# Kernel optimization log

Measured on AMD Instinct MI355X. Metric: run time of the kernel, lower is better.

Reference implementation:

```python
import jax, jax.numpy as jnp
import numpy as np

B, T, C, H = 4, 2048, 1024, 16
D = C // H  # head_size = 64


def setup_inputs() -> dict:
    key = jax.random.key(0)
    k1, k2, k3 = jax.random.split(key, 3)
    h = jax.random.normal(k1, (B, T, C), dtype=jnp.float32)
    # additive float mask, [B,1,1,T]; zeros = no padding
    attention_mask = jnp.zeros((B, 1, 1, T), dtype=jnp.float32)
    # learned params (bias=False linears), scaled like default torch init
    w_attn = jax.random.normal(k2, (C, 3 * C), dtype=jnp.float32) / np.sqrt(C)
    w_proj = jax.random.normal(k3, (C, C), dtype=jnp.float32) / np.sqrt(C)
    return {"h": h, "attention_mask": attention_mask, "w_attn": w_attn, "w_proj": w_proj}


def reference(h, attention_mask, w_attn, w_proj):
    # fused QKV projection: [B,T,3C]
    qkv = jnp.einsum("btc,cd->btd", h, w_attn)
    q, k, v = jnp.split(qkv, 3, axis=-1)
    # [B,T,C] -> [B,H,T,D]
    def to_heads(x):
        return x.reshape(B, T, H, D).transpose(0, 2, 1, 3)
    q, k, v = to_heads(q), to_heads(k), to_heads(v)
    # scaled dot-product attention with additive mask (non-causal)
    scale = 1.0 / np.sqrt(D).astype(np.float32)
    scores = jnp.einsum("bhqd,bhkd->bhqk", q, k) * scale + attention_mask
    probs = jax.nn.softmax(scores, axis=-1)
    y = jnp.einsum("bhqk,bhkd->bhqd", probs, v)
    # [B,H,T,D] -> [B,T,C]
    y = y.transpose(0, 2, 1, 3).reshape(B, T, C)
    return jnp.einsum("btc,cd->btd", y, w_proj)
```

## Files before the change

### kernel.cpp

```cpp
#include <hip/hip_runtime.h>
#include <hip/hip_bf16.h>

#define DEV static __device__ __forceinline__

typedef __attribute__((ext_vector_type(4))) float f32x4;
typedef __attribute__((ext_vector_type(8))) short bf16x8;

constexpr int Bb = 4, Ts = 2048, Cc = 1024, Hh = 16, Dd = 64;
constexpr int Mm = Bb * Ts;
constexpr float SCQ = 0.18033688f;

union frag_u {
  bf16x8 f;
  uint2  u2[2];
  ushort us[8];
  uint4  u4;
};

DEV ushort f2bf(float x) {
  union { float f; unsigned u; } v; v.f = x;
  unsigned r = v.u + 0x7FFFu + ((v.u >> 16) & 1u);
  return (ushort)(r >> 16);
}

DEV ushort f2bf_hw(float x) {
  union { __hip_bfloat16 b; ushort u; } cv;
  cv.b = __float2bfloat16(x);
  return cv.u;
}

typedef const __attribute__((address_space(1))) unsigned int gu32;
typedef __attribute__((address_space(3))) unsigned int lu32;
DEV void gload16(const void* g, void* l) {
  __builtin_amdgcn_global_load_lds((gu32*)g, (lu32*)l, 16, 0, 0);
}

DEV void ld_frag16(frag_u& fr, const ushort* lds, int row, int chunk) {
  int off = row * 128 + ((chunk ^ (row & 7)) << 4);
  fr.u4 = *reinterpret_cast<const uint4*>(reinterpret_cast<const char*>(lds) + off);
}
DEV void lds_st64p(ushort* lds, int row, int p, uint2 v) {
  int off = row * 128 + ((((p >> 3) ^ (row & 7)) << 4) | ((2 * p) & 15));
  *reinterpret_cast<uint2*>(reinterpret_cast<char*>(lds) + off) = v;
}

__global__ __launch_bounds__(256) void cvt_kernel(const float* __restrict__ in,
                                                  ushort* __restrict__ out, int n4) {
  for (int i = blockIdx.x * blockDim.x + threadIdx.x; i < n4;
       i += gridDim.x * blockDim.x) {
    float4 v = reinterpret_cast<const float4*>(in)[i];
    ushort4 o;
    o.x = f2bf(v.x); o.y = f2bf(v.y); o.z = f2bf(v.z); o.w = f2bf(v.w);
    reinterpret_cast<ushort4*>(out)[i] = o;
  }
}

__global__ __launch_bounds__(256) void transpose_cvt(const float* __restrict__ in,
                                                     ushort* __restrict__ out,
                                                     int R, int Ccols) {
  __shared__ float tile[32][33];
  int c0 = blockIdx.x * 32, r0 = blockIdx.y * 32;
  int tx = threadIdx.x & 31, ty = threadIdx.x >> 5;
#pragma unroll
  for (int i = 0; i < 4; ++i) {
    int r = ty + i * 8;
    tile[r][tx] = in[(size_t)(r0 + r) * Ccols + c0 + tx];
  }
  __syncthreads();
#pragma unroll
  for (int i = 0; i < 4; ++i) {
    int r = ty + i * 8;
    out[(size_t)(c0 + r) * R + r0 + tx] = f2bf(tile[tx][r]);
  }
}

__global__ __launch_bounds__(512, 2) void gemm256_qkv(const ushort* __restrict__ A,
                                                      const ushort* __restrict__ Bt,
                                                      ushort* __restrict__ Qb,
                                                      ushort* __restrict__ Kb,
                                                      ushort* __restrict__ Vb,
                                                      const float* __restrict__ maskp) {
  __shared__ ushort Lds[2][4][128 * 64];
  const int tid = threadIdx.x;
  const int lane = tid & 63, wid = tid >> 6;
  const int g = lane >> 4, l15 = lane & 15;
  const int wm = wid >> 2, wn = wid & 3;

  const int flat = blockIdx.y * 12 + blockIdx.x;
  const int swz = (flat & 7) * 48 + (flat >> 3);
  const int bx = swz % 12, by = swz / 12;
  const int m0 = by * 256, n0 = bx * 256;
  constexpr int K = 1024, nkt = K / 64;

#define STAGE(slot, region, gbase, gRow0, kt)                                   \
  {                                                                             \
    _Pragma("unroll") for (int i = 0; i < 2; ++i) {                             \
      int q = wid * 128 + i * 64 + lane;                                        \
      int row = q >> 3, c = (q & 7) ^ (row & 7);                                \
      gload16((gbase) + (size_t)((gRow0) + row) * K + (kt) * 64 + c * 8,        \
              &Lds[slot][region][(size_t)(wid * 128 + i * 64) * 8]);            \
    }                                                                           \
  }

  f32x4 acc[8][4];
#pragma unroll
  for (int i = 0; i < 8; ++i)
#pragma unroll
    for (int j = 0; j < 4; ++j) acc[i][j] = f32x4{0.f, 0.f, 0.f, 0.f};

  STAGE(0, 0, A, m0, 0);
  STAGE(0, 1, A, m0 + 128, 0);
  STAGE(0, 2, Bt, n0, 0);
  STAGE(0, 3, Bt, n0 + 128, 0);
  STAGE(1, 2, Bt, n0, 1);
  STAGE(1, 3, Bt, n0 + 128, 1);
  asm volatile("s_waitcnt vmcnt(4)" ::: "memory");
  __builtin_amdgcn_s_barrier();

  frag_u bf[4][2];
  for (int t = 0; t < nkt; ++t) {
    const int s = t & 1;
    const ushort* Acur = Lds[s][wm];
    const ushort* Bcur = Lds[s][2 + (wn >> 1)];
    const int browb = (wn & 1) * 64;

#pragma unroll
    for (int p = 0; p < 4; ++p) {
      frag_u af[2][2];
#pragma unroll
      for (int m2 = 0; m2 < 2; ++m2)
#pragma unroll
        for (int ks = 0; ks < 2; ++ks)
          ld_frag16(af[m2][ks], Acur, (2 * p + m2) * 16 + l15, 4 * ks + g);
      if (p == 0) {
#pragma unroll
        for (int n = 0; n < 4; ++n)
#pragma unroll
          for (int ks = 0; ks < 2; ++ks)
            ld_frag16(bf[n][ks], Bcur, browb + n * 16 + l15, 4 * ks + g);
        if (t + 1 < nkt) STAGE((t + 1) & 1, 0, A, m0, t + 1);
      }
      if (p == 1 && t + 2 < nkt) STAGE(s, 2, Bt, n0, t + 2);
      if (p == 2 && t + 1 < nkt) STAGE((t + 1) & 1, 1, A, m0 + 128, t + 1);
      if (p == 3 && t + 2 < nkt) STAGE(s, 3, Bt, n0 + 128, t + 2);

      __builtin_amdgcn_s_barrier();
      asm volatile("s_waitcnt lgkmcnt(0)" ::: "memory");
      __builtin_amdgcn_sched_barrier(0);
      __builtin_amdgcn_s_setprio(1);
#pragma unroll
      for (int m2 = 0; m2 < 2; ++m2)
#pragma unroll
        for (int n = 0; n < 4; ++n)
#pragma unroll
          for (int ks = 0; ks < 2; ++ks)
            acc[2 * p + m2][n] = __builtin_amdgcn_mfma_f32_16x16x32_bf16(
                af[m2][ks].f, bf[n][ks].f, acc[2 * p + m2][n], 0, 0, 0);
      __builtin_amdgcn_s_setprio(0);
      __builtin_amdgcn_sched_barrier(0);
      if (p == 3) asm volatile("s_waitcnt vmcnt(2)" ::: "memory");
      __builtin_amdgcn_s_barrier();
    }
  }
#undef STAGE

  asm volatile("s_waitcnt vmcnt(0)" ::: "memory");

  const int seg = bx >> 2;
  ushort* dst = (seg == 0) ? Qb : (seg == 1) ? Kb : Vb;
#pragma unroll
  for (int mi = 0; mi < 8; ++mi) {
#pragma unroll
    for (int r = 0; r < 4; ++r) {
      int mrow = m0 + wm * 128 + mi * 16 + 4 * g + r;
      int b = mrow >> 11, tt = mrow & 2047;
      float vs = (seg == 2) ? __expf(maskp[(size_t)b * Ts + tt])
                            : (seg == 0 ? SCQ : 1.f);
#pragma unroll
      for (int n = 0; n < 4; ++n) {
        int col = (bx & 3) * 256 + wn * 64 + n * 16 + l15;
        int hd = col >> 6, d = col & 63;
        size_t idx = (seg == 2)
            ? (((size_t)(b * Hh + hd)) * Dd + d) * Ts + tt
            : (((size_t)(b * Hh + hd)) * Ts + tt) * Dd + d;
        dst[idx] = f2bf(acc[mi][n][r] * vs);
      }
    }
  }
}

__global__ __launch_bounds__(256) void gemm_bt(const ushort* __restrict__ A,
                                               const ushort* __restrict__ Bt,
                                               int M, int N, int K,
                                               float* __restrict__ Cf) {
  __shared__ ushort Al[2][128 * 64];
  __shared__ ushort Bl[2][128 * 64];
  const int tid = threadIdx.x;
  const int lane = tid & 63, wid = tid >> 6;
  const int g = lane >> 4, l15 = lane & 15;
  const int wr = wid >> 1, wc = wid & 1;
  const int m0 = blockIdx.y * 128, n0 = blockIdx.x * 128;

#define ISSUE(slot, kt)                                                         \
  {                                                                             \
    _Pragma("unroll") for (int it = 0; it < 4; ++it) {                          \
      int chunk = wid * 256 + it * 64 + lane;                                   \
      int row = chunk >> 3, c16 = (chunk & 7) ^ (row & 7);                      \
      gload16(A + (size_t)(m0 + row) * K + (kt) * 64 + c16 * 8,                 \
              Al[slot] + (size_t)(wid * 256 + it * 64) * 8);                    \
      gload16(Bt + (size_t)(n0 + row) * K + (kt) * 64 + c16 * 8,                \
              Bl[slot] + (size_t)(wid * 256 + it * 64) * 8);                    \
    }                                                                           \
  }

  f32x4 acc[4][4];
#pragma unroll
  for (int i = 0; i < 4; ++i)
#pragma unroll
    for (int j = 0; j < 4; ++j) acc[i][j] = f32x4{0.f, 0.f, 0.f, 0.f};

  const int nkt = K >> 6;
  ISSUE(0, 0);
  __syncthreads();
  for (int kt = 0; kt < nkt; ++kt) {
    const int s = kt & 1;
    if (kt + 1 < nkt) ISSUE(s ^ 1, kt + 1);
#pragma unroll
    for (int ks = 0; ks < 2; ++ks) {
      frag_u af[4], bfr[4];
#pragma unroll
      for (int i = 0; i < 4; ++i) {
        ld_frag16(af[i], Al[s], wr * 64 + i * 16 + l15, 4 * ks + g);
        ld_frag16(bfr[i], Bl[s], wc * 64 + i * 16 + l15, 4 * ks + g);
      }
#pragma unroll
      for (int i = 0; i < 4; ++i)
#pragma unroll
        for (int j = 0; j < 4; ++j)
          acc[i][j] = __builtin_amdgcn_mfma_f32_16x16x32_bf16(af[i].f, bfr[j].f,
                                                              acc[i][j], 0, 0, 0);
    }
    __syncthreads();
  }
#undef ISSUE

#pragma unroll
  for (int i = 0; i < 4; ++i)
#pragma unroll
    for (int j = 0; j < 4; ++j) {
      int mrow = m0 + wr * 64 + i * 16 + 4 * g;
      int ncol = n0 + wc * 64 + j * 16 + l15;
#pragma unroll
      for (int r = 0; r < 4; ++r)
        Cf[(size_t)(mrow + r) * N + ncol] = acc[i][j][r];
    }
}

__global__ __launch_bounds__(512, 4) void attn_kernel(const ushort* __restrict__ Qb,
                                                      const ushort* __restrict__ Kb,
                                                      const ushort* __restrict__ VTb,
                                                      const float* __restrict__ mask,
                                                      ushort* __restrict__ Yb) {
  __shared__ ushort Klds[2][64 * 64];
  __shared__ ushort Vlds[2][64 * 64];
  __shared__ ushort wlds[2][64];

  const int tid = threadIdx.x;
  const int lane = tid & 63, wid = tid >> 6;
  const int g = lane >> 4, l15 = lane & 15;
  const int bh = blockIdx.x;
  const int b = bh >> 4, h = bh & 15;
  const int qt = blockIdx.y;

  const ushort* Qh = Qb + (size_t)bh * Ts * Dd;
  const ushort* Kh = Kb + (size_t)bh * Ts * Dd;
  const ushort* Vh = VTb + (size_t)bh * Dd * Ts;
  const float* mrow = mask + (size_t)b * Ts;

  const int krow = tid >> 3, kpos = tid & 7;
  const int kc16 = kpos ^ (krow & 7);
  const int srow = tid >> 3, sc16 = tid & 7;
  const int vp0 = 32 * (sc16 >> 2) + 16 * (sc16 & 1) + 4 * ((sc16 >> 1) & 1);
  const int wp = (tid & 32) | ((tid & 12) << 1) | ((tid & 16) >> 2) | (tid & 3);

  frag_u aq[2][2];
#pragma unroll
  for (int qsub = 0; qsub < 2; ++qsub) {
    const ushort* qp = Qh + (size_t)(qt * 256 + wid * 32 + qsub * 16 + l15) * Dd;
#pragma unroll
    for (int ks = 0; ks < 2; ++ks)
      aq[qsub][ks].u4 = *reinterpret_cast<const uint4*>(qp + ks * 32 + 8 * g);
  }

  f32x4 acc[2][4];
  f32x4 lacc[2];
#pragma unroll
  for (int q = 0; q < 2; ++q) {
    lacc[q] = f32x4{0.f, 0.f, 0.f, 0.f};
#pragma unroll
    for (int dt = 0; dt < 4; ++dt) acc[q][dt] = f32x4{0.f, 0.f, 0.f, 0.f};
  }

  uint4 vreg;
  float wreg = 0.f;

#define ISSUE(kt, buf)                                                          \
  gload16(Kh + (size_t)((kt) * 64 + krow) * Dd + kc16 * 8,                      \
          Klds[buf] + (size_t)(wid * 64) * 8);                                  \
  vreg = *reinterpret_cast<const uint4*>(Vh + (size_t)srow * Ts + (kt) * 64 + sc16 * 8); \
  wreg = (tid < 64) ? __expf(mrow[(kt) * 64 + tid]) : 0.f;

#define COMMIT(buf)                                                             \
  lds_st64p(Vlds[buf], srow, vp0, uint2{vreg.x, vreg.y});                       \
  lds_st64p(Vlds[buf], srow, vp0 + 8, uint2{vreg.z, vreg.w});                   \
  if (tid < 64) wlds[buf][wp] = f2bf_hw(wreg);

  ISSUE(0, 0);
  COMMIT(0);
  __syncthreads();

  const int NT = Ts / 64;
  for (int kt = 0; kt < NT; ++kt) {
    const int cur = kt & 1;
    const bool more = (kt + 1 < NT);
    if (more) { ISSUE(kt + 1, cur ^ 1); }

    f32x4 s[2][4];
#pragma unroll
    for (int q = 0; q < 2; ++q)
#pragma unroll
      for (int n = 0; n < 4; ++n) s[q][n] = f32x4{0.f, 0.f, 0.f, 0.f};
    __builtin_amdgcn_s_setprio(1);
#pragma unroll
    for (int ks = 0; ks < 2; ++ks)
#pragma unroll
      for (int n = 0; n < 4; ++n) {
        frag_u bk;
        ld_frag16(bk, Klds[cur], n * 16 + l15, 4 * ks + g);
#pragma unroll
        for (int q = 0; q < 2; ++q)
          s[q][n] = __builtin_amdgcn_mfma_f32_16x16x32_bf16(bk.f, aq[q][ks].f,
                                                            s[q][n], 0, 0, 0);
      }
    __builtin_amdgcn_s_setprio(0);

    frag_u pa[2][2];
#pragma unroll
    for (int q = 0; q < 2; ++q)
#pragma unroll
      for (int n = 0; n < 4; ++n)
#pragma unroll
        for (int r = 0; r < 4; ++r)
          pa[q][n >> 1].us[(n & 1) * 4 + r] =
              f2bf_hw(__builtin_amdgcn_exp2f(s[q][n][r]));

    frag_u wf[2];
    wf[0].u4 = *reinterpret_cast<const uint4*>(&wlds[cur][8 * g]);
    wf[1].u4 = *reinterpret_cast<const uint4*>(&wlds[cur][32 + 8 * g]);
    __builtin_amdgcn_s_setprio(1);
#pragma unroll
    for (int ks = 0; ks < 2; ++ks)
#pragma unroll
      for (int q = 0; q < 2; ++q)
        lacc[q] = __builtin_amdgcn_mfma_f32_16x16x32_bf16(pa[q][ks].f, wf[ks].f,
                                                          lacc[q], 0, 0, 0);
#pragma unroll
    for (int ks = 0; ks < 2; ++ks)
#pragma unroll
      for (int dt = 0; dt < 4; ++dt) {
        frag_u bv;
        ld_frag16(bv, Vlds[cur], dt * 16 + l15, 4 * ks + g);
#pragma unroll
        for (int q = 0; q < 2; ++q)
          acc[q][dt] = __builtin_amdgcn_mfma_f32_16x16x32_bf16(pa[q][ks].f, bv.f,
                                                               acc[q][dt], 0, 0, 0);
      }
    __builtin_amdgcn_s_setprio(0);

    if (more) { COMMIT(cur ^ 1); }
    __syncthreads();
  }
#undef ISSUE
#undef COMMIT

#pragma unroll
  for (int q = 0; q < 2; ++q) {
#pragma unroll
    for (int r = 0; r < 4; ++r) {
      float inv = 1.0f / lacc[q][r];
      int t = qt * 256 + wid * 32 + q * 16 + 4 * g + r;
      size_t base = ((size_t)(b * Ts + t)) * Cc + h * Dd;
#pragma unroll
      for (int dt = 0; dt < 4; ++dt)
        Yb[base + dt * 16 + l15] = f2bf(acc[q][dt][r] * inv);
    }
  }
}

extern "C" void kernel_launch(void* const* d_in, const int* in_sizes, int n_in,
                              void* d_out, int out_size, void* d_ws, size_t ws_size,
                              hipStream_t stream) {
  const float* h    = (const float*)d_in[0];
  const float* mask = (const float*)d_in[1];
  const float* wa   = (const float*)d_in[2];
  const float* wp   = (const float*)d_in[3];
  float* out = (float*)d_out;

  char* ws = (char*)d_ws;
  ushort* hbf     = (ushort*)(ws);
  ushort* wattn_t = (ushort*)(ws + (16u << 20));
  ushort* wproj_t = (ushort*)(ws + (22u << 20));
  ushort* Qb      = (ushort*)(ws + (24u << 20));
  ushort* Kb      = (ushort*)(ws + (40u << 20));
  ushort* VTb     = (ushort*)(ws + (56u << 20));
  ushort* Ybf = hbf;

  cvt_kernel<<<2048, 256, 0, stream>>>(h, hbf, (Mm * Cc) / 4);
  transpose_cvt<<<dim3(3 * Cc / 32, Cc / 32), 256, 0, stream>>>(wa, wattn_t, Cc, 3 * Cc);
  transpose_cvt<<<dim3(Cc / 32, Cc / 32), 256, 0, stream>>>(wp, wproj_t, Cc, Cc);

  gemm256_qkv<<<dim3(12, 32), 512, 0, stream>>>(hbf, wattn_t, Qb, Kb, VTb, mask);

  attn_kernel<<<dim3(Bb * Hh, Ts / 256), 512, 0, stream>>>(Qb, Kb, VTb, mask, Ybf);

  gemm_bt<<<dim3(Cc / 128, Mm / 128), 256, 0, stream>>>(
      Ybf, wproj_t, Mm, Cc, Cc, out);
}
```

Before: 199.0 us.

## Precompute exp(mask) once and rebalance QKV GEMM prefetch schedule

Adds a small kernel that computes exp(mask) once, so the QKV GEMM epilogue and the attention inner loop read precomputed values instead of evaluating exp repeatedly. The QKV GEMM pipeline is also restructured: both A halves are staged in phases 0-1 and both B halves in phases 2-3. Loads are now issued unconditionally, with clamped tile indices in the tail, and the vmcnt waits are retuned to 8 and 6. This keeps the per-wave outstanding load count uniform, at the cost of redundant tail loads and one extra kernel launch.

```diff
diff --git a/kernel.cpp b/kernel.cpp
--- a/kernel.cpp
+++ b/kernel.cpp
@@ -55,6 +55,12 @@
   }
 }
 
+__global__ __launch_bounds__(256) void expmask_kernel(const float* __restrict__ m,
+                                                      float* __restrict__ em, int n) {
+  int i = blockIdx.x * blockDim.x + threadIdx.x;
+  if (i < n) em[i] = __expf(m[i]);
+}
+
 __global__ __launch_bounds__(256) void transpose_cvt(const float* __restrict__ in,
                                                      ushort* __restrict__ out,
                                                      int R, int Ccols) {
@@ -79,7 +85,7 @@
                                                       ushort* __restrict__ Qb,
                                                       ushort* __restrict__ Kb,
                                                       ushort* __restrict__ Vb,
-                                                      const float* __restrict__ maskp) {
+                                                      const float* __restrict__ expm) {
   __shared__ ushort Lds[2][4][128 * 64];
   const int tid = threadIdx.x;
   const int lane = tid & 63, wid = tid >> 6;
@@ -120,6 +126,9 @@
   frag_u bf[4][2];
   for (int t = 0; t < nkt; ++t) {
     const int s = t & 1;
+    const int sN = s ^ 1;
+    const int tA = (t + 1 < nkt) ? t + 1 : nkt - 1;
+    const int tB = (t + 2 < nkt) ? t + 2 : nkt - 1;
     const ushort* Acur = Lds[s][wm];
     const ushort* Bcur = Lds[s][2 + (wn >> 1)];
     const int browb = (wn & 1) * 64;
@@ -138,11 +147,11 @@
 #pragma unroll
           for (int ks = 0; ks < 2; ++ks)
             ld_frag16(bf[n][ks], Bcur, browb + n * 16 + l15, 4 * ks + g);
-        if (t + 1 < nkt) STAGE((t + 1) & 1, 0, A, m0, t + 1);
+        STAGE(sN, 0, A, m0, tA);
       }
-      if (p == 1 && t + 2 < nkt) STAGE(s, 2, Bt, n0, t + 2);
-      if (p == 2 && t + 1 < nkt) STAGE((t + 1) & 1, 1, A, m0 + 128, t + 1);
-      if (p == 3 && t + 2 < nkt) STAGE(s, 3, Bt, n0 + 128, t + 2);
+      if (p == 1) STAGE(sN, 1, A, m0 + 128, tA);
+      if (p == 2) STAGE(s, 2, Bt, n0, tB);
+      if (p == 3) STAGE(s, 3, Bt, n0 + 128, tB);
 
       __builtin_amdgcn_s_barrier();
       asm volatile("s_waitcnt lgkmcnt(0)" ::: "memory");
@@ -158,7 +167,8 @@
                 af[m2][ks].f, bf[n][ks].f, acc[2 * p + m2][n], 0, 0, 0);
       __builtin_amdgcn_s_setprio(0);
       __builtin_amdgcn_sched_barrier(0);
-      if (p == 3) asm volatile("s_waitcnt vmcnt(2)" ::: "memory");
+      if (p == 1) asm volatile("s_waitcnt vmcnt(8)" ::: "memory");
+      if (p == 3) asm volatile("s_waitcnt vmcnt(6)" ::: "memory");
       __builtin_amdgcn_s_barrier();
     }
   }
@@ -174,7 +184,7 @@
     for (int r = 0; r < 4; ++r) {
       int mrow = m0 + wm * 128 + mi * 16 + 4 * g + r;
       int b = mrow >> 11, tt = mrow & 2047;
-      float vs = (seg == 2) ? __expf(maskp[(size_t)b * Ts + tt])
+      float vs = (seg == 2) ? expm[(size_t)b * Ts + tt]
                             : (seg == 0 ? SCQ : 1.f);
 #pragma unroll
       for (int n = 0; n < 4; ++n) {
@@ -259,7 +269,7 @@
 __global__ __launch_bounds__(512, 4) void attn_kernel(const ushort* __restrict__ Qb,
                                                       const ushort* __restrict__ Kb,
                                                       const ushort* __restrict__ VTb,
-                                                      const float* __restrict__ mask,
+                                                      const float* __restrict__ expm,
                                                       ushort* __restrict__ Yb) {
   __shared__ ushort Klds[2][64 * 64];
   __shared__ ushort Vlds[2][64 * 64];
@@ -275,7 +285,7 @@
   const ushort* Qh = Qb + (size_t)bh * Ts * Dd;
   const ushort* Kh = Kb + (size_t)bh * Ts * Dd;
   const ushort* Vh = VTb + (size_t)bh * Dd * Ts;
-  const float* mrow = mask + (size_t)b * Ts;
+  const float* erow = expm + (size_t)b * Ts;
 
   const int krow = tid >> 3, kpos = tid & 7;
   const int kc16 = kpos ^ (krow & 7);
@@ -308,7 +318,7 @@
   gload16(Kh + (size_t)((kt) * 64 + krow) * Dd + kc16 * 8,                      \
           Klds[buf] + (size_t)(wid * 64) * 8);                                  \
   vreg = *reinterpret_cast<const uint4*>(Vh + (size_t)srow * Ts + (kt) * 64 + sc16 * 8); \
-  wreg = (tid < 64) ? __expf(mrow[(kt) * 64 + tid]) : 0.f;
+  wreg = (tid < 64) ? erow[(kt) * 64 + tid] : 0.f;
 
 #define COMMIT(buf)                                                             \
   lds_st64p(Vlds[buf], srow, vp0, uint2{vreg.x, vreg.y});                       \
@@ -413,15 +423,17 @@
   ushort* Qb      = (ushort*)(ws + (24u << 20));
   ushort* Kb      = (ushort*)(ws + (40u << 20));
   ushort* VTb     = (ushort*)(ws + (56u << 20));
+  float*  expm    = (float*)(ws + (72u << 20));
   ushort* Ybf = hbf;
 
   cvt_kernel<<<2048, 256, 0, stream>>>(h, hbf, (Mm * Cc) / 4);
+  expmask_kernel<<<(Bb * Ts + 255) / 256, 256, 0, stream>>>(mask, expm, Bb * Ts);
   transpose_cvt<<<dim3(3 * Cc / 32, Cc / 32), 256, 0, stream>>>(wa, wattn_t, Cc, 3 * Cc);
   transpose_cvt<<<dim3(Cc / 32, Cc / 32), 256, 0, stream>>>(wp, wproj_t, Cc, Cc);
 
-  gemm256_qkv<<<dim3(12, 32), 512, 0, stream>>>(hbf, wattn_t, Qb, Kb, VTb, mask);
-
-  attn_kernel<<<dim3(Bb * Hh, Ts / 256), 512, 0, stream>>>(Qb, Kb, VTb, mask, Ybf);
+  gemm256_qkv<<<dim3(12, 32), 512, 0, stream>>>(hbf, wattn_t, Qb, Kb, VTb, expm);
+
+  attn_kernel<<<dim3(Bb * Hh, Ts / 256), 512, 0, stream>>>(Qb, Kb, VTb, expm, Ybf);
 
   gemm_bt<<<dim3(Cc / 128, Mm / 128), 256, 0, stream>>>(
       Ybf, wproj_t, Mm, Cc, Cc, out);
```

After: 203.9 us. 2.5% more time.
